# Performance work log

Measured on AMD Instinct MI355X. Metric: run time of the kernel, lower is better.

The kernel has to match this reference:

```python
import jax, jax.numpy as jnp
import numpy as np

DIM, WIDTH = 5, 64
BATCH, N_SAVE = 4096, 64
RTOL, ATOL = 1e-3, 1e-6
SAFETY, FMIN, FMAX = 0.9, 0.2, 10.0
MAX_STEPS, DT0, EPS = 64, 0.1, 1e-6

# Tsit5 (Tsitouras 2011) Butcher tableau
A21 = 0.161
A31, A32 = -0.008480655492356989, 0.335480655492357
A41, A42, A43 = 2.8971530571054935, -6.359448489975075, 4.3622954328695815
A51, A52, A53, A54 = 5.325864828439257, -11.748883564062828, 7.4955393428898365, -0.09249506636175525
A61, A62, A63, A64, A65 = 5.86145544294642, -12.92096931784711, 8.159367898576159, -0.071584973281401, -0.028269050394068383
B1, B2, B3, B4, B5, B6 = 0.09646076681806523, 0.01, 0.4798896504144996, 1.379008574103742, -3.290069515436081, 2.324710524099774
# embedded 4th-order error coefficients (b - bhat)
E1, E2, E3, E4, E5, E6, E7 = (-0.00178001105222577714, -0.0008164344596567469,
    0.007880878010261995, -0.1447110071732629, 0.5823571654525552,
    -0.45808210592918697, 0.015151515151515152)


def _mlp(y, W1, b1, W2, b2, W3, b3, W4, b4):
    # eqx.nn.MLP(5, 5, width 64, depth 3, softplus)
    h = jax.nn.softplus(y @ W1.T + b1)
    h = jax.nn.softplus(h @ W2.T + b2)
    h = jax.nn.softplus(h @ W3.T + b3)
    return h @ W4.T + b4


def _solve_one(y0, t_eval, params):
    f = lambda y: _mlp(y, *params)
    t0, t1 = t_eval[0], t_eval[-1]
    # save points at/before t0 get y0
    ys0 = jnp.where((t_eval <= t0 + EPS)[:, None], y0[None, :], 0.0)

    def body(carry, _):
        t, y, h, ys = carry
        done = t >= t1 - EPS
        hc = jnp.where(done, 0.0, jnp.minimum(h, t1 - t))  # clip last step to t1
        k1 = f(y)
        k2 = f(y + hc * (A21 * k1))
        k3 = f(y + hc * (A31 * k1 + A32 * k2))
        k4 = f(y + hc * (A41 * k1 + A42 * k2 + A43 * k3))
        k5 = f(y + hc * (A51 * k1 + A52 * k2 + A53 * k3 + A54 * k4))
        k6 = f(y + hc * (A61 * k1 + A62 * k2 + A63 * k3 + A64 * k4 + A65 * k5))
        ynew = y + hc * (B1 * k1 + B2 * k2 + B3 * k3 + B4 * k4 + B5 * k5 + B6 * k6)
        k7 = f(ynew)  # FSAL stage, also used for error + interpolation
        err = hc * (E1 * k1 + E2 * k2 + E3 * k3 + E4 * k4 + E5 * k5 + E6 * k6 + E7 * k7)
        scale = ATOL + RTOL * jnp.maximum(jnp.abs(y), jnp.abs(ynew))
        enorm = jnp.sqrt(jnp.mean((err / scale) ** 2))
        enorm_c = jax.lax.stop_gradient(jnp.maximum(enorm, 1e-10))
        accept = enorm <= 1.0
        factor = jnp.clip(SAFETY * enorm_c ** -0.2, FMIN, FMAX)  # I-controller, order 5
        step_ok = accept & ~done
        t_next = jnp.where(step_ok, t + hc, t)
        y_next = jnp.where(step_ok, ynew, y)
        h_next = jnp.where(done, h, hc * factor)
        # cubic Hermite interpolation for save points inside (t, t_next]
        s = ((t_eval - t) / jnp.maximum(hc, 1e-12))[:, None]
        h00 = 2 * s**3 - 3 * s**2 + 1
        h10 = s**3 - 2 * s**2 + s
        h01 = -2 * s**3 + 3 * s**2
        h11 = s**3 - s**2
        yi = h00 * y + h10 * hc * k1 + h01 * ynew + h11 * hc * k7
        mask = (t_eval > t) & (t_eval <= t_next + EPS) & step_ok
        ys = jnp.where(mask[:, None], yi, ys)
        return (t_next, y_next, h_next, ys), None

    h0 = jnp.asarray(DT0, dtype=y0.dtype)
    (_, _, _, ys), _ = jax.lax.scan(body, (t0, y0, h0, ys0), None, length=MAX_STEPS)
    return ys  # [N_SAVE, DIM]


def setup_inputs() -> dict:
    key = jax.random.key(0)
    ks = jax.random.split(key, 9)
    y0 = jax.random.normal(ks[0], (BATCH, DIM), dtype=jnp.float32)
    t_eval = jnp.linspace(0.0, 1.0, N_SAVE, dtype=jnp.float32)

    def lin(k, out_d, in_d):
        lim = 1.0 / np.sqrt(in_d)
        kw, kb = jax.random.split(k)
        W = jax.random.uniform(kw, (out_d, in_d), jnp.float32, -lim, lim)
        b = jax.random.uniform(kb, (out_d,), jnp.float32, -lim, lim)
        return W, b

    W1, b1 = lin(ks[1], WIDTH, DIM)
    W2, b2 = lin(ks[2], WIDTH, WIDTH)
    W3, b3 = lin(ks[3], WIDTH, WIDTH)
    W4, b4 = lin(ks[4], DIM, WIDTH)
    return {"y0": y0, "t_eval": t_eval, "W1": W1, "b1": b1, "W2": W2, "b2": b2,
            "W3": W3, "b3": b3, "W4": W4, "b4": b4}


def reference(y0, t_eval, W1, b1, W2, b2, W3, b3, W4, b4):
    params = (W1, b1, W2, b2, W3, b3, W4, b4)
    return jax.vmap(lambda y: _solve_one(y, t_eval, params))(y0)  # [BATCH, N_SAVE, DIM]
```

## Files before the change

kernel.cpp:

```cpp
#include <hip/hip_runtime.h>
#include <cmath>

namespace {

constexpr int kDim = 5;
constexpr int kSave = 64;
constexpr int kTraj = 16;
constexpr int kThreads = 256;
constexpr int kMaxSteps = 64;
constexpr int ZS = 40;
constexpr int HS = 72;
constexpr int SD = 8;

typedef _Float16 half8 __attribute__((ext_vector_type(8)));
typedef float f32x4 __attribute__((ext_vector_type(4)));

__device__ __forceinline__ float softplusf(float x) {
  return fmaxf(x, 0.0f) + __logf(1.0f + __expf(-fabsf(x)));
}

__global__ __launch_bounds__(kThreads, 1)
void node_tsit5_kernel(const float* __restrict__ gy0,
                       const float* __restrict__ gte,
                       const float* __restrict__ gW1, const float* __restrict__ gb1,
                       const float* __restrict__ gW2, const float* __restrict__ gb2,
                       const float* __restrict__ gW3, const float* __restrict__ gb3,
                       const float* __restrict__ gW4, const float* __restrict__ gb4,
                       float* __restrict__ out) {
  const float A21 = 0.161f;
  const float A31 = -0.008480655492356989f, A32 = 0.335480655492357f;
  const float A41 = 2.8971530571054935f, A42 = -6.359448489975075f, A43 = 4.3622954328695815f;
  const float A51 = 5.325864828439257f, A52 = -11.748883564062828f, A53 = 7.4955393428898365f,
              A54 = -0.09249506636175525f;
  const float A61 = 5.86145544294642f, A62 = -12.92096931784711f, A63 = 8.159367898576159f,
              A64 = -0.071584973281401f, A65 = -0.028269050394068383f;
  const float B1 = 0.09646076681806523f, B2 = 0.01f, B3 = 0.4798896504144996f,
              B4 = 1.379008574103742f, B5 = -3.290069515436081f, B6 = 2.324710524099774f;
  const float E1 = -0.00178001105222577714f, E2 = -0.0008164344596567469f,
              E3 = 0.007880878010261995f, E4 = -0.1447110071732629f, E5 = 0.5823571654525552f,
              E6 = -0.45808210592918697f, E7 = 0.015151515151515152f;

  __shared__ __align__(16) _Float16 zb[kTraj * ZS];
  __shared__ __align__(16) _Float16 hiA[kTraj * HS], loA[kTraj * HS];
  __shared__ __align__(16) _Float16 hiB[kTraj * HS], loB[kTraj * HS];
  __shared__ float sTe[kSave];
  __shared__ float sY[kTraj * SD], sYN[kTraj * SD], sK1[kTraj * SD], sK7[kTraj * SD];
  __shared__ float sesq[kTraj * SD];
  __shared__ float s_hc[kTraj], s_tOld[kTraj], s_tn[kTraj];
  __shared__ int s_ok[kTraj], s_done[kTraj];

  const int tid = threadIdx.x;
  const int bid = blockIdx.x;
  const int w = tid >> 6;
  const int ln = tid & 63;
  const int quad = ln >> 4;
  const int col = ln & 15;
  const int row0 = quad * 4;
  const int nn = (w << 4) | col;
  const bool cact = col < kDim;
  const bool w0 = (w == 0);

  half8 w1c, w2h[2], w3h[2], w4h[2];
  #pragma unroll
  for (int j = 0; j < 8; ++j) {
    int kk2 = quad * 8 + j;
    float wv = 0.0f;
    if (kk2 < 5) wv = gW1[nn * 5 + kk2];
    else if (kk2 < 10) wv = gW1[nn * 5 + (kk2 - 5)];
    w1c[j] = (_Float16)wv;
  }
  #pragma unroll
  for (int kf = 0; kf < 2; ++kf)
    #pragma unroll
    for (int j = 0; j < 8; ++j) {
      int kk2 = kf * 32 + quad * 8 + j;
      w2h[kf][j] = (_Float16)gW2[nn * 64 + kk2];
      w3h[kf][j] = (_Float16)gW3[nn * 64 + kk2];
      w4h[kf][j] = cact ? (_Float16)gW4[col * 64 + kk2] : (_Float16)0.0f;
    }
  const float c1 = gb1[nn], c2 = gb2[nn], c3 = gb3[nn];
  const float c4 = cact ? gb4[col] : 0.0f;

  for (int i = tid; i < kTraj * ZS; i += kThreads) zb[i] = (_Float16)0.0f;
  if (tid < kSave) sTe[tid] = gte[tid];
  if (tid < kTraj * kDim) {
    int t = tid & 15, d = tid >> 4;
    float v = gy0[(size_t)(bid * kTraj + t) * kDim + d];
    sY[t * SD + d] = v;
    _Float16 hi = (_Float16)v;
    zb[t * ZS + d] = hi;
    zb[t * ZS + d + 5] = (_Float16)(v - (float)hi);
  }
  {
    float* ob = out + (size_t)bid * kTraj * kSave * kDim;
    for (int idx = tid; idx < kTraj * kSave * kDim; idx += kThreads) ob[idx] = 0.0f;
  }
  __syncthreads();

  const float t0v = sTe[0];
  const float t1v = sTe[kSave - 1];

  f32x4 syr, synr, kk[7];
  if (cact) {
    #pragma unroll
    for (int r = 0; r < 4; ++r)
      syr[r] = gy0[(size_t)(bid * kTraj + row0 + r) * kDim + col];
  }

  {
    int tt = tid & 15, gg = tid >> 4;
    float yv[kDim];
    #pragma unroll
    for (int d = 0; d < kDim; ++d) yv[d] = sY[tt * SD + d];
    #pragma unroll
    for (int q = 0; q < 4; ++q) {
      int n = 4 * gg + q;
      if (sTe[n] <= t0v + 1e-6f) {
        float* op = out + ((size_t)(bid * kTraj + tt) * kSave + n) * kDim;
        #pragma unroll
        for (int d = 0; d < kDim; ++d) op[d] = yv[d];
      }
    }
  }

  auto evalF = [&]() -> f32x4 {
    {
      half8 az = *(const half8*)(zb + col * ZS + quad * 8);
      f32x4 a = {c1, c1, c1, c1};
      a = __builtin_amdgcn_mfma_f32_16x16x32_f16(az, w1c, a, 0, 0, 0);
      #pragma unroll
      for (int r = 0; r < 4; ++r) {
        float s = softplusf(a[r]);
        _Float16 hi = (_Float16)s;
        hiA[(row0 + r) * HS + nn] = hi;
        loA[(row0 + r) * HS + nn] = (_Float16)(s - (float)hi);
      }
    }
    __syncthreads();
    {
      half8 ah0 = *(const half8*)(hiA + col * HS + quad * 8);
      half8 ah1 = *(const half8*)(hiA + col * HS + 32 + quad * 8);
      half8 al0 = *(const half8*)(loA + col * HS + quad * 8);
      half8 al1 = *(const half8*)(loA + col * HS + 32 + quad * 8);
      f32x4 a = {c2, c2, c2, c2};
      a = __builtin_amdgcn_mfma_f32_16x16x32_f16(ah0, w2h[0], a, 0, 0, 0);
      a = __builtin_amdgcn_mfma_f32_16x16x32_f16(ah1, w2h[1], a, 0, 0, 0);
      a = __builtin_amdgcn_mfma_f32_16x16x32_f16(al0, w2h[0], a, 0, 0, 0);
      a = __builtin_amdgcn_mfma_f32_16x16x32_f16(al1, w2h[1], a, 0, 0, 0);
      #pragma unroll
      for (int r = 0; r < 4; ++r) {
        float s = softplusf(a[r]);
        _Float16 hi = (_Float16)s;
        hiB[(row0 + r) * HS + nn] = hi;
        loB[(row0 + r) * HS + nn] = (_Float16)(s - (float)hi);
      }
    }
    __syncthreads();
    {
      half8 ah0 = *(const half8*)(hiB + col * HS + quad * 8);
      half8 ah1 = *(const half8*)(hiB + col * HS + 32 + quad * 8);
      half8 al0 = *(const half8*)(loB + col * HS + quad * 8);
      half8 al1 = *(const half8*)(loB + col * HS + 32 + quad * 8);
      f32x4 a = {c3, c3, c3, c3};
      a = __builtin_amdgcn_mfma_f32_16x16x32_f16(ah0, w3h[0], a, 0, 0, 0);
      a = __builtin_amdgcn_mfma_f32_16x16x32_f16(ah1, w3h[1], a, 0, 0, 0);
      a = __builtin_amdgcn_mfma_f32_16x16x32_f16(al0, w3h[0], a, 0, 0, 0);
      a = __builtin_amdgcn_mfma_f32_16x16x32_f16(al1, w3h[1], a, 0, 0, 0);
      #pragma unroll
      for (int r = 0; r < 4; ++r) {
        float s = softplusf(a[r]);
        _Float16 hi = (_Float16)s;
        hiA[(row0 + r) * HS + nn] = hi;
        loA[(row0 + r) * HS + nn] = (_Float16)(s - (float)hi);
      }
    }
    __syncthreads();
    f32x4 a = {c4, c4, c4, c4};
    {
      half8 ah0 = *(const half8*)(hiA + col * HS + quad * 8);
      half8 ah1 = *(const half8*)(hiA + col * HS + 32 + quad * 8);
      half8 al0 = *(const half8*)(loA + col * HS + quad * 8);
      half8 al1 = *(const half8*)(loA + col * HS + 32 + quad * 8);
      a = __builtin_amdgcn_mfma_f32_16x16x32_f16(ah0, w4h[0], a, 0, 0, 0);
      a = __builtin_amdgcn_mfma_f32_16x16x32_f16(ah1, w4h[1], a, 0, 0, 0);
      a = __builtin_amdgcn_mfma_f32_16x16x32_f16(al0, w4h[0], a, 0, 0, 0);
      a = __builtin_amdgcn_mfma_f32_16x16x32_f16(al1, w4h[1], a, 0, 0, 0);
    }
    return a;
  };

  auto zwrite = [&](f32x4 z) {
    if (w0 && cact) {
      #pragma unroll
      for (int r = 0; r < 4; ++r) {
        _Float16 hi = (_Float16)z[r];
        zb[(row0 + r) * ZS + col] = hi;
        zb[(row0 + r) * ZS + col + 5] = (_Float16)(z[r] - (float)hi);
      }
    }
    __syncthreads();
  };

  kk[0] = evalF();
  __syncthreads();

  float tcur = t0v, hcur = 0.1f;

  for (int step = 0; step < kMaxSteps; ++step) {
    if (ln < kTraj) {
      int dn = tcur >= t1v - 1e-6f;
      float hc = dn ? 0.0f : fminf(hcur, t1v - tcur);
      if (w0) { s_done[ln] = dn; s_hc[ln] = hc; s_tOld[ln] = tcur; }
    }
    __syncthreads();
    if (__ballot(s_done[ln & 15]) == ~0ull) break;

    f32x4 hcr;
    #pragma unroll
    for (int r = 0; r < 4; ++r) hcr[r] = s_hc[row0 + r];

    f32x4 z;
    #pragma unroll
    for (int r = 0; r < 4; ++r) z[r] = fmaf(hcr[r], A21 * kk[0][r], syr[r]);
    zwrite(z); kk[1] = evalF();

    #pragma unroll
    for (int r = 0; r < 4; ++r)
      z[r] = fmaf(hcr[r], fmaf(A32, kk[1][r], A31 * kk[0][r]), syr[r]);
    zwrite(z); kk[2] = evalF();

    #pragma unroll
    for (int r = 0; r < 4; ++r)
      z[r] = fmaf(hcr[r], fmaf(A43, kk[2][r], fmaf(A42, kk[1][r], A41 * kk[0][r])), syr[r]);
    zwrite(z); kk[3] = evalF();

    #pragma unroll
    for (int r = 0; r < 4; ++r)
      z[r] = fmaf(hcr[r], fmaf(A54, kk[3][r], fmaf(A53, kk[2][r],
                  fmaf(A52, kk[1][r], A51 * kk[0][r]))), syr[r]);
    zwrite(z); kk[4] = evalF();

    #pragma unroll
    for (int r = 0; r < 4; ++r)
      z[r] = fmaf(hcr[r], fmaf(A65, kk[4][r], fmaf(A64, kk[3][r], fmaf(A63, kk[2][r],
                  fmaf(A62, kk[1][r], A61 * kk[0][r])))), syr[r]);
    zwrite(z); kk[5] = evalF();

    #pragma unroll
    for (int r = 0; r < 4; ++r)
      synr[r] = fmaf(hcr[r], fmaf(B6, kk[5][r], fmaf(B5, kk[4][r], fmaf(B4, kk[3][r],
                 fmaf(B3, kk[2][r], fmaf(B2, kk[1][r], B1 * kk[0][r]))))), syr[r]);
    zwrite(synr); kk[6] = evalF();

    if (w0 && cact) {
      #pragma unroll
      for (int r = 0; r < 4; ++r) {
        float err = hcr[r] * fmaf(E7, kk[6][r], fmaf(E6, kk[5][r], fmaf(E5, kk[4][r],
                    fmaf(E4, kk[3][r], fmaf(E3, kk[2][r], fmaf(E2, kk[1][r], E1 * kk[0][r]))))));
        float sc = fmaf(1e-3f, fmaxf(fabsf(syr[r]), fabsf(synr[r])), 1e-6f);
        float rr = err / sc;
        int o = (row0 + r) * SD + col;
        sesq[o] = rr * rr;
        sYN[o] = synr[r];
        sK1[o] = kk[0][r];
        sK7[o] = kk[6][r];
      }
    }
    __syncthreads();
    if (ln < kTraj) {
      float s = 0.0f;
      #pragma unroll
      for (int d = 0; d < kDim; ++d) s += sesq[ln * SD + d];
      float enorm = sqrtf(s / 5.0f);
      float enc = fmaxf(enorm, 1e-10f);
      int accept = enorm <= 1.0f;
      float factor = fminf(fmaxf(0.9f * powf(enc, -0.2f), 0.2f), 10.0f);
      int dn = s_done[ln];
      int ok = accept && !dn;
      float hc = s_hc[ln];
      float tn = ok ? tcur + hc : tcur;
      if (w0) { s_tn[ln] = tn; s_ok[ln] = ok; }
      tcur = tn;
      hcur = dn ? hcur : hc * factor;
    }
    __syncthreads();
    {
      int tt = tid & 15, gg = tid >> 4;
      if (s_ok[tt]) {
        float tOld = s_tOld[tt], hcs = s_hc[tt], tNew = s_tn[tt];
        float inv = 1.0f / fmaxf(hcs, 1e-12f);
        float yv[kDim], ynv[kDim], k1v[kDim], k7v[kDim];
        #pragma unroll
        for (int d = 0; d < kDim; ++d) {
          yv[d] = sY[tt * SD + d];
          ynv[d] = sYN[tt * SD + d];
          k1v[d] = hcs * sK1[tt * SD + d];
          k7v[d] = hcs * sK7[tt * SD + d];
        }
        #pragma unroll
        for (int q = 0; q < 4; ++q) {
          int n = 4 * gg + q;
          float te = sTe[n];
          if (te > tOld && te <= tNew + 1e-6f) {
            float sx = (te - tOld) * inv;
            float s2 = sx * sx, s3 = s2 * sx;
            float h00 = 2.f * s3 - 3.f * s2 + 1.f;
            float h10 = s3 - 2.f * s2 + sx;
            float h01 = -2.f * s3 + 3.f * s2;
            float h11 = s3 - s2;
            float* op = out + ((size_t)(bid * kTraj + tt) * kSave + n) * kDim;
            #pragma unroll
            for (int d = 0; d < kDim; ++d)
              op[d] = h00 * yv[d] + h10 * k1v[d] + h01 * ynv[d] + h11 * k7v[d];
          }
        }
      }
    }
    __syncthreads();
    if (cact) {
      #pragma unroll
      for (int r = 0; r < 4; ++r) {
        int ok = s_ok[row0 + r];
        syr[r] = ok ? synr[r] : syr[r];
        kk[0][r] = ok ? kk[6][r] : kk[0][r];
        if (w0) sY[(row0 + r) * SD + col] = syr[r];
      }
    }
    __syncthreads();
  }
}

}

extern "C" void kernel_launch(void* const* d_in, const int* in_sizes, int n_in,
                              void* d_out, int out_size, void* d_ws, size_t ws_size,
                              hipStream_t stream) {
  const float* y0 = (const float*)d_in[0];
  const float* te = (const float*)d_in[1];
  const float* W1 = (const float*)d_in[2];
  const float* b1 = (const float*)d_in[3];
  const float* W2 = (const float*)d_in[4];
  const float* b2 = (const float*)d_in[5];
  const float* W3 = (const float*)d_in[6];
  const float* b3 = (const float*)d_in[7];
  const float* W4 = (const float*)d_in[8];
  const float* b4 = (const float*)d_in[9];
  float* out = (float*)d_out;

  const int batch = in_sizes[0] / kDim;
  const int blocks = batch / kTraj;
  hipLaunchKernelGGL(node_tsit5_kernel, dim3(blocks), dim3(kThreads), 0, stream,
                     y0, te, W1, b1, W2, b2, W3, b3, W4, b4, out);
}
```

Before: 109.4 us.

## Replicate per-wave ODE state and replace block barriers with wave-local LDS fences

Each of the four waves now holds its own copy of the stage input buffer, trajectory state and step controller, so the error norm is reduced with cross-lane shuffles and step acceptance is decided in registers instead of through shared memory. This removes roughly five block-wide barriers per step outside the MLP layers, replacing them with wave-local s_waitcnt fences, and distributes the dense-output writes across waves by save index. The layer-2/3/4 MFMAs are split into two independent accumulator chains (hi and lo parts) to shorten dependency latency. The costs are more LDS, redundant per-wave controller arithmetic, and fast exp/log in place of powf for the step factor. Correctness relies on all waves computing identical step decisions.

```diff
diff --git a/kernel.cpp b/kernel.cpp
--- a/kernel.cpp
+++ b/kernel.cpp
@@ -17,6 +17,10 @@
 
 __device__ __forceinline__ float softplusf(float x) {
   return fmaxf(x, 0.0f) + __logf(1.0f + __expf(-fabsf(x)));
+}
+
+__device__ __forceinline__ void lds_fence() {
+  asm volatile("s_waitcnt lgkmcnt(0)" ::: "memory");
 }
 
 __global__ __launch_bounds__(kThreads, 1)
@@ -40,14 +44,13 @@
               E3 = 0.007880878010261995f, E4 = -0.1447110071732629f, E5 = 0.5823571654525552f,
               E6 = -0.45808210592918697f, E7 = 0.015151515151515152f;
 
-  __shared__ __align__(16) _Float16 zb[kTraj * ZS];
-  __shared__ __align__(16) _Float16 hiA[kTraj * HS], loA[kTraj * HS];
-  __shared__ __align__(16) _Float16 hiB[kTraj * HS], loB[kTraj * HS];
-  __shared__ float sTe[kSave];
-  __shared__ float sY[kTraj * SD], sYN[kTraj * SD], sK1[kTraj * SD], sK7[kTraj * SD];
-  __shared__ float sesq[kTraj * SD];
-  __shared__ float s_hc[kTraj], s_tOld[kTraj], s_tn[kTraj];
-  __shared__ int s_ok[kTraj], s_done[kTraj];
+  __shared__ __align__(16) _Float16 zbp[4][kTraj * ZS];
+  __shared__ __align__(16) _Float16 h0[kTraj * HS], l0[kTraj * HS];
+  __shared__ __align__(16) _Float16 h1[kTraj * HS], l1[kTraj * HS];
+  __shared__ __align__(16) _Float16 h2[kTraj * HS], l2[kTraj * HS];
+  __shared__ __align__(16) float ySs[4][kTraj * SD], ynS[4][kTraj * SD];
+  __shared__ __align__(16) float k1S[4][kTraj * SD], k7S[4][kTraj * SD];
+  __shared__ float ctT[4][kTraj], ctH[4][kTraj], ctN[4][kTraj], ctO[4][kTraj];
 
   const int tid = threadIdx.x;
   const int bid = blockIdx.x;
@@ -58,7 +61,6 @@
   const int row0 = quad * 4;
   const int nn = (w << 4) | col;
   const bool cact = col < kDim;
-  const bool w0 = (w == 0);
 
   half8 w1c, w2h[2], w3h[2], w4h[2];
   #pragma unroll
@@ -81,227 +83,251 @@
   const float c1 = gb1[nn], c2 = gb2[nn], c3 = gb3[nn];
   const float c4 = cact ? gb4[col] : 0.0f;
 
-  for (int i = tid; i < kTraj * ZS; i += kThreads) zb[i] = (_Float16)0.0f;
-  if (tid < kSave) sTe[tid] = gte[tid];
-  if (tid < kTraj * kDim) {
-    int t = tid & 15, d = tid >> 4;
-    float v = gy0[(size_t)(bid * kTraj + t) * kDim + d];
-    sY[t * SD + d] = v;
-    _Float16 hi = (_Float16)v;
-    zb[t * ZS + d] = hi;
-    zb[t * ZS + d + 5] = (_Float16)(v - (float)hi);
+  const float t0v = gte[0];
+  const float t1v = gte[kSave - 1];
+  float teq[4];
+  #pragma unroll
+  for (int q = 0; q < 4; ++q) teq[q] = gte[16 * w + 4 * quad + q];
+
+  for (int i = ln; i < kTraj * ZS; i += 64) zbp[w][i] = (_Float16)0.0f;
+
+  f32x4 syr = {0, 0, 0, 0}, synr = {0, 0, 0, 0}, kk[7];
+  if (cact) {
+    #pragma unroll
+    for (int r = 0; r < 4; ++r) {
+      float v = gy0[(size_t)(bid * kTraj + row0 + r) * kDim + col];
+      syr[r] = v;
+      _Float16 hi = (_Float16)v;
+      zbp[w][(row0 + r) * ZS + col] = hi;
+      zbp[w][(row0 + r) * ZS + col + 5] = (_Float16)(v - (float)hi);
+      ySs[w][(row0 + r) * SD + col] = v;
+    }
   }
+  lds_fence();
+
   {
-    float* ob = out + (size_t)bid * kTraj * kSave * kDim;
-    for (int idx = tid; idx < kTraj * kSave * kDim; idx += kThreads) ob[idx] = 0.0f;
+    int tt = ln & 15;
+    float y0v[kDim];
+    #pragma unroll
+    for (int d = 0; d < kDim; ++d) y0v[d] = ySs[w][tt * SD + d];
+    #pragma unroll
+    for (int q = 0; q < 4; ++q) {
+      int n = 16 * w + 4 * quad + q;
+      bool isy0 = teq[q] <= t0v + 1e-6f;
+      float* op = out + ((size_t)(bid * kTraj + tt) * kSave + n) * kDim;
+      #pragma unroll
+      for (int d = 0; d < kDim; ++d) op[d] = isy0 ? y0v[d] : 0.0f;
+    }
   }
-  __syncthreads();
-
-  const float t0v = sTe[0];
-  const float t1v = sTe[kSave - 1];
-
-  f32x4 syr, synr, kk[7];
-  if (cact) {
-    #pragma unroll
-    for (int r = 0; r < 4; ++r)
-      syr[r] = gy0[(size_t)(bid * kTraj + row0 + r) * kDim + col];
-  }
-
-  {
-    int tt = tid & 15, gg = tid >> 4;
-    float yv[kDim];
-    #pragma unroll
-    for (int d = 0; d < kDim; ++d) yv[d] = sY[tt * SD + d];
-    #pragma unroll
-    for (int q = 0; q < 4; ++q) {
-      int n = 4 * gg + q;
-      if (sTe[n] <= t0v + 1e-6f) {
-        float* op = out + ((size_t)(bid * kTraj + tt) * kSave + n) * kDim;
-        #pragma unroll
-        for (int d = 0; d < kDim; ++d) op[d] = yv[d];
-      }
-    }
-  }
 
   auto evalF = [&]() -> f32x4 {
     {
-      half8 az = *(const half8*)(zb + col * ZS + quad * 8);
+      half8 az = *(const half8*)(zbp[w] + col * ZS + quad * 8);
       f32x4 a = {c1, c1, c1, c1};
       a = __builtin_amdgcn_mfma_f32_16x16x32_f16(az, w1c, a, 0, 0, 0);
       #pragma unroll
       for (int r = 0; r < 4; ++r) {
         float s = softplusf(a[r]);
         _Float16 hi = (_Float16)s;
-        hiA[(row0 + r) * HS + nn] = hi;
-        loA[(row0 + r) * HS + nn] = (_Float16)(s - (float)hi);
+        h0[(row0 + r) * HS + nn] = hi;
+        l0[(row0 + r) * HS + nn] = (_Float16)(s - (float)hi);
       }
     }
     __syncthreads();
     {
-      half8 ah0 = *(const half8*)(hiA + col * HS + quad * 8);
-      half8 ah1 = *(const half8*)(hiA + col * HS + 32 + quad * 8);
-      half8 al0 = *(const half8*)(loA + col * HS + quad * 8);
-      half8 al1 = *(const half8*)(loA + col * HS + 32 + quad * 8);
+      half8 ah0 = *(const half8*)(h0 + col * HS + quad * 8);
+      half8 ah1 = *(const half8*)(h0 + col * HS + 32 + quad * 8);
+      half8 al0 = *(const half8*)(l0 + col * HS + quad * 8);
+      half8 al1 = *(const half8*)(l0 + col * HS + 32 + quad * 8);
       f32x4 a = {c2, c2, c2, c2};
+      f32x4 b = {0, 0, 0, 0};
       a = __builtin_amdgcn_mfma_f32_16x16x32_f16(ah0, w2h[0], a, 0, 0, 0);
+      b = __builtin_amdgcn_mfma_f32_16x16x32_f16(al0, w2h[0], b, 0, 0, 0);
       a = __builtin_amdgcn_mfma_f32_16x16x32_f16(ah1, w2h[1], a, 0, 0, 0);
-      a = __builtin_amdgcn_mfma_f32_16x16x32_f16(al0, w2h[0], a, 0, 0, 0);
-      a = __builtin_amdgcn_mfma_f32_16x16x32_f16(al1, w2h[1], a, 0, 0, 0);
+      b = __builtin_amdgcn_mfma_f32_16x16x32_f16(al1, w2h[1], b, 0, 0, 0);
+      a += b;
       #pragma unroll
       for (int r = 0; r < 4; ++r) {
         float s = softplusf(a[r]);
         _Float16 hi = (_Float16)s;
-        hiB[(row0 + r) * HS + nn] = hi;
-        loB[(row0 + r) * HS + nn] = (_Float16)(s - (float)hi);
+        h1[(row0 + r) * HS + nn] = hi;
+        l1[(row0 + r) * HS + nn] = (_Float16)(s - (float)hi);
       }
     }
     __syncthreads();
     {
-      half8 ah0 = *(const half8*)(hiB + col * HS + quad * 8);
-      half8 ah1 = *(const half8*)(hiB + col * HS + 32 + quad * 8);
-      half8 al0 = *(const half8*)(loB + col * HS + quad * 8);
-      half8 al1 = *(const half8*)(loB + col * HS + 32 + quad * 8);
+      half8 ah0 = *(const half8*)(h1 + col * HS + quad * 8);
+      half8 ah1 = *(const half8*)(h1 + col * HS + 32 + quad * 8);
+      half8 al0 = *(const half8*)(l1 + col * HS + quad * 8);
+      half8 al1 = *(const half8*)(l1 + col * HS + 32 + quad * 8);
       f32x4 a = {c3, c3, c3, c3};
+      f32x4 b = {0, 0, 0, 0};
       a = __builtin_amdgcn_mfma_f32_16x16x32_f16(ah0, w3h[0], a, 0, 0, 0);
+      b = __builtin_amdgcn_mfma_f32_16x16x32_f16(al0, w3h[0], b, 0, 0, 0);
       a = __builtin_amdgcn_mfma_f32_16x16x32_f16(ah1, w3h[1], a, 0, 0, 0);
-      a = __builtin_amdgcn_mfma_f32_16x16x32_f16(al0, w3h[0], a, 0, 0, 0);
-      a = __builtin_amdgcn_mfma_f32_16x16x32_f16(al1, w3h[1], a, 0, 0, 0);
+      b = __builtin_amdgcn_mfma_f32_16x16x32_f16(al1, w3h[1], b, 0, 0, 0);
+      a += b;
       #pragma unroll
       for (int r = 0; r < 4; ++r) {
         float s = softplusf(a[r]);
         _Float16 hi = (_Float16)s;
-        hiA[(row0 + r) * HS + nn] = hi;
-        loA[(row0 + r) * HS + nn] = (_Float16)(s - (float)hi);
+        h2[(row0 + r) * HS + nn] = hi;
+        l2[(row0 + r) * HS + nn] = (_Float16)(s - (float)hi);
       }
     }
     __syncthreads();
     f32x4 a = {c4, c4, c4, c4};
     {
-      half8 ah0 = *(const half8*)(hiA + col * HS + quad * 8);
-      half8 ah1 = *(const half8*)(hiA + col * HS + 32 + quad * 8);
-      half8 al0 = *(const half8*)(loA + col * HS + quad * 8);
-      half8 al1 = *(const half8*)(loA + col * HS + 32 + quad * 8);
+      half8 ah0 = *(const half8*)(h2 + col * HS + quad * 8);
+      half8 ah1 = *(const half8*)(h2 + col * HS + 32 + quad * 8);
+      half8 al0 = *(const half8*)(l2 + col * HS + quad * 8);
+      half8 al1 = *(const half8*)(l2 + col * HS + 32 + quad * 8);
+      f32x4 b = {0, 0, 0, 0};
       a = __builtin_amdgcn_mfma_f32_16x16x32_f16(ah0, w4h[0], a, 0, 0, 0);
+      b = __builtin_amdgcn_mfma_f32_16x16x32_f16(al0, w4h[0], b, 0, 0, 0);
       a = __builtin_amdgcn_mfma_f32_16x16x32_f16(ah1, w4h[1], a, 0, 0, 0);
-      a = __builtin_amdgcn_mfma_f32_16x16x32_f16(al0, w4h[0], a, 0, 0, 0);
-      a = __builtin_amdgcn_mfma_f32_16x16x32_f16(al1, w4h[1], a, 0, 0, 0);
+      b = __builtin_amdgcn_mfma_f32_16x16x32_f16(al1, w4h[1], b, 0, 0, 0);
+      a += b;
     }
     return a;
   };
 
   auto zwrite = [&](f32x4 z) {
-    if (w0 && cact) {
+    if (cact) {
       #pragma unroll
       for (int r = 0; r < 4; ++r) {
         _Float16 hi = (_Float16)z[r];
-        zb[(row0 + r) * ZS + col] = hi;
-        zb[(row0 + r) * ZS + col + 5] = (_Float16)(z[r] - (float)hi);
-      }
-    }
-    __syncthreads();
+        zbp[w][(row0 + r) * ZS + col] = hi;
+        zbp[w][(row0 + r) * ZS + col + 5] = (_Float16)(z[r] - (float)hi);
+      }
+    }
+    lds_fence();
   };
 
   kk[0] = evalF();
-  __syncthreads();
-
-  float tcur = t0v, hcur = 0.1f;
+
+  f32x4 tcur = {t0v, t0v, t0v, t0v};
+  f32x4 hcur = {0.1f, 0.1f, 0.1f, 0.1f};
 
   for (int step = 0; step < kMaxSteps; ++step) {
-    if (ln < kTraj) {
-      int dn = tcur >= t1v - 1e-6f;
-      float hc = dn ? 0.0f : fminf(hcur, t1v - tcur);
-      if (w0) { s_done[ln] = dn; s_hc[ln] = hc; s_tOld[ln] = tcur; }
-    }
-    __syncthreads();
-    if (__ballot(s_done[ln & 15]) == ~0ull) break;
-
-    f32x4 hcr;
-    #pragma unroll
-    for (int r = 0; r < 4; ++r) hcr[r] = s_hc[row0 + r];
+    f32x4 hcs, tOldr;
+    bool dnr[4];
+    bool all4 = true;
+    #pragma unroll
+    for (int r = 0; r < 4; ++r) {
+      bool d = tcur[r] >= t1v - 1e-6f;
+      dnr[r] = d;
+      all4 &= d;
+      hcs[r] = d ? 0.0f : fminf(hcur[r], t1v - tcur[r]);
+      tOldr[r] = tcur[r];
+    }
+    if (__ballot(all4) == ~0ull) break;
 
     f32x4 z;
     #pragma unroll
-    for (int r = 0; r < 4; ++r) z[r] = fmaf(hcr[r], A21 * kk[0][r], syr[r]);
+    for (int r = 0; r < 4; ++r) z[r] = fmaf(hcs[r], A21 * kk[0][r], syr[r]);
     zwrite(z); kk[1] = evalF();
 
     #pragma unroll
     for (int r = 0; r < 4; ++r)
-      z[r] = fmaf(hcr[r], fmaf(A32, kk[1][r], A31 * kk[0][r]), syr[r]);
+      z[r] = fmaf(hcs[r], fmaf(A32, kk[1][r], A31 * kk[0][r]), syr[r]);
     zwrite(z); kk[2] = evalF();
 
     #pragma unroll
     for (int r = 0; r < 4; ++r)
-      z[r] = fmaf(hcr[r], fmaf(A43, kk[2][r], fmaf(A42, kk[1][r], A41 * kk[0][r])), syr[r]);
+      z[r] = fmaf(hcs[r], fmaf(A43, kk[2][r], fmaf(A42, kk[1][r], A41 * kk[0][r])), syr[r]);
     zwrite(z); kk[3] = evalF();
 
     #pragma unroll
     for (int r = 0; r < 4; ++r)
-      z[r] = fmaf(hcr[r], fmaf(A54, kk[3][r], fmaf(A53, kk[2][r],
+      z[r] = fmaf(hcs[r], fmaf(A54, kk[3][r], fmaf(A53, kk[2][r],
                   fmaf(A52, kk[1][r], A51 * kk[0][r]))), syr[r]);
     zwrite(z); kk[4] = evalF();
 
     #pragma unroll
     for (int r = 0; r < 4; ++r)
-      z[r] = fmaf(hcr[r], fmaf(A65, kk[4][r], fmaf(A64, kk[3][r], fmaf(A63, kk[2][r],
+      z[r] = fmaf(hcs[r], fmaf(A65, kk[4][r], fmaf(A64, kk[3][r], fmaf(A63, kk[2][r],
                   fmaf(A62, kk[1][r], A61 * kk[0][r])))), syr[r]);
     zwrite(z); kk[5] = evalF();
 
     #pragma unroll
     for (int r = 0; r < 4; ++r)
-      synr[r] = fmaf(hcr[r], fmaf(B6, kk[5][r], fmaf(B5, kk[4][r], fmaf(B4, kk[3][r],
+      synr[r] = fmaf(hcs[r], fmaf(B6, kk[5][r], fmaf(B5, kk[4][r], fmaf(B4, kk[3][r],
                  fmaf(B3, kk[2][r], fmaf(B2, kk[1][r], B1 * kk[0][r]))))), syr[r]);
     zwrite(synr); kk[6] = evalF();
 
-    if (w0 && cact) {
-      #pragma unroll
-      for (int r = 0; r < 4; ++r) {
-        float err = hcr[r] * fmaf(E7, kk[6][r], fmaf(E6, kk[5][r], fmaf(E5, kk[4][r],
-                    fmaf(E4, kk[3][r], fmaf(E3, kk[2][r], fmaf(E2, kk[1][r], E1 * kk[0][r]))))));
-        float sc = fmaf(1e-3f, fmaxf(fabsf(syr[r]), fabsf(synr[r])), 1e-6f);
-        float rr = err / sc;
+    f32x4 rr2;
+    #pragma unroll
+    for (int r = 0; r < 4; ++r) {
+      float err = hcs[r] * fmaf(E7, kk[6][r], fmaf(E6, kk[5][r], fmaf(E5, kk[4][r],
+                  fmaf(E4, kk[3][r], fmaf(E3, kk[2][r], fmaf(E2, kk[1][r], E1 * kk[0][r]))))));
+      float sc = fmaf(1e-3f, fmaxf(fabsf(syr[r]), fabsf(synr[r])), 1e-6f);
+      float rr = err / sc;
+      rr2[r] = cact ? rr * rr : 0.0f;
+    }
+    #pragma unroll
+    for (int m = 1; m < 16; m <<= 1) {
+      #pragma unroll
+      for (int r = 0; r < 4; ++r) rr2[r] += __shfl_xor(rr2[r], m, 64);
+    }
+
+    bool okr[4];
+    #pragma unroll
+    for (int r = 0; r < 4; ++r) {
+      float enorm = __fsqrt_rn(rr2[r] * 0.2f);
+      float enc = fmaxf(enorm, 1e-10f);
+      bool accept = enorm <= 1.0f;
+      float factor = fminf(fmaxf(0.9f * __expf(-0.2f * __logf(enc)), 0.2f), 10.0f);
+      bool ok = accept && !dnr[r];
+      okr[r] = ok;
+      tcur[r] = ok ? tcur[r] + hcs[r] : tcur[r];
+      hcur[r] = dnr[r] ? hcur[r] : hcs[r] * factor;
+    }
+
+    if (cact) {
+      #pragma unroll
+      for (int r = 0; r < 4; ++r) {
         int o = (row0 + r) * SD + col;
-        sesq[o] = rr * rr;
-        sYN[o] = synr[r];
-        sK1[o] = kk[0][r];
-        sK7[o] = kk[6][r];
-      }
-    }
-    __syncthreads();
-    if (ln < kTraj) {
-      float s = 0.0f;
-      #pragma unroll
-      for (int d = 0; d < kDim; ++d) s += sesq[ln * SD + d];
-      float enorm = sqrtf(s / 5.0f);
-      float enc = fmaxf(enorm, 1e-10f);
-      int accept = enorm <= 1.0f;
-      float factor = fminf(fmaxf(0.9f * powf(enc, -0.2f), 0.2f), 10.0f);
-      int dn = s_done[ln];
-      int ok = accept && !dn;
-      float hc = s_hc[ln];
-      float tn = ok ? tcur + hc : tcur;
-      if (w0) { s_tn[ln] = tn; s_ok[ln] = ok; }
-      tcur = tn;
-      hcur = dn ? hcur : hc * factor;
-    }
-    __syncthreads();
-    {
-      int tt = tid & 15, gg = tid >> 4;
-      if (s_ok[tt]) {
-        float tOld = s_tOld[tt], hcs = s_hc[tt], tNew = s_tn[tt];
-        float inv = 1.0f / fmaxf(hcs, 1e-12f);
+        ySs[w][o] = syr[r];
+        ynS[w][o] = synr[r];
+        k1S[w][o] = kk[0][r];
+        k7S[w][o] = kk[6][r];
+      }
+    }
+    if (col == 0) {
+      #pragma unroll
+      for (int r = 0; r < 4; ++r) {
+        int m = row0 + r;
+        ctT[w][m] = tOldr[r];
+        ctH[w][m] = hcs[r];
+        ctN[w][m] = tcur[r];
+        ctO[w][m] = okr[r] ? 1.0f : 0.0f;
+      }
+    }
+    lds_fence();
+
+    {
+      int tt = ln & 15;
+      if (ctO[w][tt] != 0.0f) {
+        float tOld = ctT[w][tt], hcv = ctH[w][tt], tNew = ctN[w][tt];
+        float inv = 1.0f / fmaxf(hcv, 1e-12f);
+        const float* yb = &ySs[w][tt * SD];
+        const float* nb = &ynS[w][tt * SD];
+        const float* ab = &k1S[w][tt * SD];
+        const float* bb = &k7S[w][tt * SD];
         float yv[kDim], ynv[kDim], k1v[kDim], k7v[kDim];
         #pragma unroll
         for (int d = 0; d < kDim; ++d) {
-          yv[d] = sY[tt * SD + d];
-          ynv[d] = sYN[tt * SD + d];
-          k1v[d] = hcs * sK1[tt * SD + d];
-          k7v[d] = hcs * sK7[tt * SD + d];
+          yv[d] = yb[d];
+          ynv[d] = nb[d];
+          k1v[d] = hcv * ab[d];
+          k7v[d] = hcv * bb[d];
         }
         #pragma unroll
         for (int q = 0; q < 4; ++q) {
-          int n = 4 * gg + q;
-          float te = sTe[n];
+          float te = teq[q];
           if (te > tOld && te <= tNew + 1e-6f) {
+            int n = 16 * w + 4 * quad + q;
             float sx = (te - tOld) * inv;
             float s2 = sx * sx, s3 = s2 * sx;
             float h00 = 2.f * s3 - 3.f * s2 + 1.f;
@@ -316,17 +342,11 @@
         }
       }
     }
-    __syncthreads();
-    if (cact) {
-      #pragma unroll
-      for (int r = 0; r < 4; ++r) {
-        int ok = s_ok[row0 + r];
-        syr[r] = ok ? synr[r] : syr[r];
-        kk[0][r] = ok ? kk[6][r] : kk[0][r];
-        if (w0) sY[(row0 + r) * SD + col] = syr[r];
-      }
-    }
-    __syncthreads();
+
+    #pragma unroll
+    for (int r = 0; r < 4; ++r) {
+      if (okr[r]) { syr[r] = synr[r]; kk[0][r] = kk[6][r]; }
+    }
   }
 }
 
```

Measured after the change: 110.6 us. No clear change (+1.1%).

## Use per-wave stage input buffers, triple-buffer hidden layers, split MFMA accumulators

Applied to the files above, without the earlier changes.

Each wavefront now writes its own copy of the stage input into a private shared-memory buffer, so the block-wide barrier after each input write goes away. The hidden-layer buffers become three distinct sets, which removes the write-after-read hazard between layers 1 and 3 and drops the barrier after the first evaluation. The hi and lo MFMA products go into two independent accumulators that are summed at the end, which shortens the dependent MFMA chain. The cost is more shared memory and redundant input writes from every wave.

```diff
diff --git a/kernel.cpp b/kernel.cpp
--- a/kernel.cpp
+++ b/kernel.cpp
@@ -40,9 +40,10 @@
               E3 = 0.007880878010261995f, E4 = -0.1447110071732629f, E5 = 0.5823571654525552f,
               E6 = -0.45808210592918697f, E7 = 0.015151515151515152f;
 
-  __shared__ __align__(16) _Float16 zb[kTraj * ZS];
-  __shared__ __align__(16) _Float16 hiA[kTraj * HS], loA[kTraj * HS];
-  __shared__ __align__(16) _Float16 hiB[kTraj * HS], loB[kTraj * HS];
+  __shared__ __align__(16) _Float16 zbp[4][kTraj * ZS];
+  __shared__ __align__(16) _Float16 h0[kTraj * HS], l0[kTraj * HS];
+  __shared__ __align__(16) _Float16 h1[kTraj * HS], l1[kTraj * HS];
+  __shared__ __align__(16) _Float16 h2[kTraj * HS], l2[kTraj * HS];
   __shared__ float sTe[kSave];
   __shared__ float sY[kTraj * SD], sYN[kTraj * SD], sK1[kTraj * SD], sK7[kTraj * SD];
   __shared__ float sesq[kTraj * SD];
@@ -81,31 +82,32 @@
   const float c1 = gb1[nn], c2 = gb2[nn], c3 = gb3[nn];
   const float c4 = cact ? gb4[col] : 0.0f;
 
-  for (int i = tid; i < kTraj * ZS; i += kThreads) zb[i] = (_Float16)0.0f;
+  for (int i = ln; i < kTraj * ZS; i += 64) zbp[w][i] = (_Float16)0.0f;
   if (tid < kSave) sTe[tid] = gte[tid];
   if (tid < kTraj * kDim) {
     int t = tid & 15, d = tid >> 4;
-    float v = gy0[(size_t)(bid * kTraj + t) * kDim + d];
-    sY[t * SD + d] = v;
-    _Float16 hi = (_Float16)v;
-    zb[t * ZS + d] = hi;
-    zb[t * ZS + d + 5] = (_Float16)(v - (float)hi);
+    sY[t * SD + d] = gy0[(size_t)(bid * kTraj + t) * kDim + d];
   }
   {
     float* ob = out + (size_t)bid * kTraj * kSave * kDim;
     for (int idx = tid; idx < kTraj * kSave * kDim; idx += kThreads) ob[idx] = 0.0f;
   }
+
+  f32x4 syr = {0, 0, 0, 0}, synr = {0, 0, 0, 0}, kk[7];
+  if (cact) {
+    #pragma unroll
+    for (int r = 0; r < 4; ++r) {
+      float v = gy0[(size_t)(bid * kTraj + row0 + r) * kDim + col];
+      syr[r] = v;
+      _Float16 hi = (_Float16)v;
+      zbp[w][(row0 + r) * ZS + col] = hi;
+      zbp[w][(row0 + r) * ZS + col + 5] = (_Float16)(v - (float)hi);
+    }
+  }
   __syncthreads();
 
   const float t0v = sTe[0];
   const float t1v = sTe[kSave - 1];
-
-  f32x4 syr, synr, kk[7];
-  if (cact) {
-    #pragma unroll
-    for (int r = 0; r < 4; ++r)
-      syr[r] = gy0[(size_t)(bid * kTraj + row0 + r) * kDim + col];
-  }
 
   {
     int tt = tid & 15, gg = tid >> 4;
@@ -125,84 +127,88 @@
 
   auto evalF = [&]() -> f32x4 {
     {
-      half8 az = *(const half8*)(zb + col * ZS + quad * 8);
+      half8 az = *(const half8*)(zbp[w] + col * ZS + quad * 8);
       f32x4 a = {c1, c1, c1, c1};
       a = __builtin_amdgcn_mfma_f32_16x16x32_f16(az, w1c, a, 0, 0, 0);
       #pragma unroll
       for (int r = 0; r < 4; ++r) {
         float s = softplusf(a[r]);
         _Float16 hi = (_Float16)s;
-        hiA[(row0 + r) * HS + nn] = hi;
-        loA[(row0 + r) * HS + nn] = (_Float16)(s - (float)hi);
-      }
-    }
-    __syncthreads();
-    {
-      half8 ah0 = *(const half8*)(hiA + col * HS + quad * 8);
-      half8 ah1 = *(const half8*)(hiA + col * HS + 32 + quad * 8);
-      half8 al0 = *(const half8*)(loA + col * HS + quad * 8);
-      half8 al1 = *(const half8*)(loA + col * HS + 32 + quad * 8);
+        h0[(row0 + r) * HS + nn] = hi;
+        l0[(row0 + r) * HS + nn] = (_Float16)(s - (float)hi);
+      }
+    }
+    __syncthreads();
+    {
+      half8 ah0 = *(const half8*)(h0 + col * HS + quad * 8);
+      half8 ah1 = *(const half8*)(h0 + col * HS + 32 + quad * 8);
+      half8 al0 = *(const half8*)(l0 + col * HS + quad * 8);
+      half8 al1 = *(const half8*)(l0 + col * HS + 32 + quad * 8);
       f32x4 a = {c2, c2, c2, c2};
+      f32x4 b = {0, 0, 0, 0};
       a = __builtin_amdgcn_mfma_f32_16x16x32_f16(ah0, w2h[0], a, 0, 0, 0);
+      b = __builtin_amdgcn_mfma_f32_16x16x32_f16(al0, w2h[0], b, 0, 0, 0);
       a = __builtin_amdgcn_mfma_f32_16x16x32_f16(ah1, w2h[1], a, 0, 0, 0);
-      a = __builtin_amdgcn_mfma_f32_16x16x32_f16(al0, w2h[0], a, 0, 0, 0);
-      a = __builtin_amdgcn_mfma_f32_16x16x32_f16(al1, w2h[1], a, 0, 0, 0);
+      b = __builtin_amdgcn_mfma_f32_16x16x32_f16(al1, w2h[1], b, 0, 0, 0);
+      a += b;
       #pragma unroll
       for (int r = 0; r < 4; ++r) {
         float s = softplusf(a[r]);
         _Float16 hi = (_Float16)s;
-        hiB[(row0 + r) * HS + nn] = hi;
-        loB[(row0 + r) * HS + nn] = (_Float16)(s - (float)hi);
-      }
-    }
-    __syncthreads();
-    {
-      half8 ah0 = *(const half8*)(hiB + col * HS + quad * 8);
-      half8 ah1 = *(const half8*)(hiB + col * HS + 32 + quad * 8);
-      half8 al0 = *(const half8*)(loB + col * HS + quad * 8);
-      half8 al1 = *(const half8*)(loB + col * HS + 32 + quad * 8);
+        h1[(row0 + r) * HS + nn] = hi;
+        l1[(row0 + r) * HS + nn] = (_Float16)(s - (float)hi);
+      }
+    }
+    __syncthreads();
+    {
+      half8 ah0 = *(const half8*)(h1 + col * HS + quad * 8);
+      half8 ah1 = *(const half8*)(h1 + col * HS + 32 + quad * 8);
+      half8 al0 = *(const half8*)(l1 + col * HS + quad * 8);
+      half8 al1 = *(const half8*)(l1 + col * HS + 32 + quad * 8);
       f32x4 a = {c3, c3, c3, c3};
+      f32x4 b = {0, 0, 0, 0};
       a = __builtin_amdgcn_mfma_f32_16x16x32_f16(ah0, w3h[0], a, 0, 0, 0);
+      b = __builtin_amdgcn_mfma_f32_16x16x32_f16(al0, w3h[0], b, 0, 0, 0);
       a = __builtin_amdgcn_mfma_f32_16x16x32_f16(ah1, w3h[1], a, 0, 0, 0);
-      a = __builtin_amdgcn_mfma_f32_16x16x32_f16(al0, w3h[0], a, 0, 0, 0);
-      a = __builtin_amdgcn_mfma_f32_16x16x32_f16(al1, w3h[1], a, 0, 0, 0);
+      b = __builtin_amdgcn_mfma_f32_16x16x32_f16(al1, w3h[1], b, 0, 0, 0);
+      a += b;
       #pragma unroll
       for (int r = 0; r < 4; ++r) {
         float s = softplusf(a[r]);
         _Float16 hi = (_Float16)s;
-        hiA[(row0 + r) * HS + nn] = hi;
-        loA[(row0 + r) * HS + nn] = (_Float16)(s - (float)hi);
+        h2[(row0 + r) * HS + nn] = hi;
+        l2[(row0 + r) * HS + nn] = (_Float16)(s - (float)hi);
       }
     }
     __syncthreads();
     f32x4 a = {c4, c4, c4, c4};
     {
-      half8 ah0 = *(const half8*)(hiA + col * HS + quad * 8);
-      half8 ah1 = *(const half8*)(hiA + col * HS + 32 + quad * 8);
-      half8 al0 = *(const half8*)(loA + col * HS + quad * 8);
-      half8 al1 = *(const half8*)(loA + col * HS + 32 + quad * 8);
+      half8 ah0 = *(const half8*)(h2 + col * HS + quad * 8);
+      half8 ah1 = *(const half8*)(h2 + col * HS + 32 + quad * 8);
+      half8 al0 = *(const half8*)(l2 + col * HS + quad * 8);
+      half8 al1 = *(const half8*)(l2 + col * HS + 32 + quad * 8);
+      f32x4 b = {0, 0, 0, 0};
       a = __builtin_amdgcn_mfma_f32_16x16x32_f16(ah0, w4h[0], a, 0, 0, 0);
+      b = __builtin_amdgcn_mfma_f32_16x16x32_f16(al0, w4h[0], b, 0, 0, 0);
       a = __builtin_amdgcn_mfma_f32_16x16x32_f16(ah1, w4h[1], a, 0, 0, 0);
-      a = __builtin_amdgcn_mfma_f32_16x16x32_f16(al0, w4h[0], a, 0, 0, 0);
-      a = __builtin_amdgcn_mfma_f32_16x16x32_f16(al1, w4h[1], a, 0, 0, 0);
+      b = __builtin_amdgcn_mfma_f32_16x16x32_f16(al1, w4h[1], b, 0, 0, 0);
+      a += b;
     }
     return a;
   };
 
   auto zwrite = [&](f32x4 z) {
-    if (w0 && cact) {
+    if (cact) {
       #pragma unroll
       for (int r = 0; r < 4; ++r) {
         _Float16 hi = (_Float16)z[r];
-        zb[(row0 + r) * ZS + col] = hi;
-        zb[(row0 + r) * ZS + col + 5] = (_Float16)(z[r] - (float)hi);
-      }
-    }
-    __syncthreads();
+        zbp[w][(row0 + r) * ZS + col] = hi;
+        zbp[w][(row0 + r) * ZS + col + 5] = (_Float16)(z[r] - (float)hi);
+      }
+    }
   };
 
   kk[0] = evalF();
-  __syncthreads();
 
   float tcur = t0v, hcur = 0.1f;
 
```

After: 111.0 us. About the same (+1.5%).
